# Optimization experiments

Measured on AMD Instinct MI355X. Metric: run time of the kernel, lower is better.

Reference implementation:

```python
import jax, jax.numpy as jnp
import numpy as np

N_ENT, N_REL, N_TRIG, N_ARGS = 100000, 250000, 50000, 250000
ENT_DIM, REL_R, RTYPE_DIM, ROLE_DIM, REL_SIZE = 288, 256, 32, 256, 200
ARG_DIM = REL_R + RTYPE_DIM + ENT_DIM  # 576


def setup_inputs() -> dict:
    key = jax.random.key(0)
    ks = jax.random.split(key, 11)
    s_in = 1.0 / np.sqrt(ARG_DIM)
    return {
        "ent_embeds": jax.random.normal(ks[0], (N_ENT, ENT_DIM), jnp.float32),
        "rel_embeds": jax.random.normal(ks[1], (N_REL, REL_R), jnp.float32),
        "rtype_table": jax.random.normal(ks[2], (REL_SIZE + 1, RTYPE_DIM), jnp.float32),
        "W_in": jax.random.normal(ks[3], (ARG_DIM, ROLE_DIM), jnp.float32) * s_in,
        "W_out": jax.random.normal(ks[4], (ARG_DIM, ROLE_DIM), jnp.float32) * s_in,
        "rtype_ids": jax.random.randint(ks[5], (N_REL,), 0, REL_SIZE, jnp.int32),
        "trig_ent_id": jax.random.randint(ks[6], (N_TRIG,), 0, N_ENT, jnp.int32),
        "arg_trig": jax.random.randint(ks[7], (N_ARGS,), 0, N_TRIG, jnp.int32),
        "arg_rel": jax.random.randint(ks[8], (N_ARGS,), 0, N_REL, jnp.int32),
        "arg_ent": jax.random.randint(ks[9], (N_ARGS,), 0, N_ENT, jnp.int32),
        "arg_is_in": jax.random.randint(ks[10], (N_ARGS,), 0, 2, jnp.int32),
    }


def reference(ent_embeds, rel_embeds, rtype_table, W_in, W_out,
              rtype_ids, trig_ent_id, arg_trig, arg_rel, arg_ent, arg_is_in):
    # per-relation type embedding (rtype_embedding_layer)
    rt_embeds = rtype_table[rtype_ids]                       # [N_REL, RTYPE_DIM]
    # per-argument gather + concat (get_arg_embeds): [rel | rtype | arg-entity]
    x = jnp.concatenate([rel_embeds[arg_rel],
                         rt_embeds[arg_rel],
                         ent_embeds[arg_ent]], axis=-1)      # [N_ARGS, ARG_DIM]
    # in_arg_layer vs out_arg_layer selected per argument (io_ids membership)
    m = arg_is_in.astype(x.dtype)[:, None]
    y = (x * m) @ W_in + (x * (1.0 - m)) @ W_out             # [N_ARGS, ROLE_DIM]
    # sum-aggregate per trigger (torch.sum over stacked arg embeds)
    args_sum = jax.ops.segment_sum(y, arg_trig, num_segments=N_TRIG)
    # concat trigger embedding with aggregated args (event_representation)
    return jnp.concatenate([ent_embeds[trig_ent_id], args_sum], axis=-1)  # [N_TRIG, ENT_DIM+ROLE_DIM]
```

## Files before the change

kernel.cpp:

```cpp
#include <hip/hip_runtime.h>
#include <hip/hip_bf16.h>
#include <stdint.h>

#define N_ENT    100000
#define N_REL    250000
#define N_TRIG   50000
#define N_ARGS   250000
#define ENT_DIM  288
#define REL_R    256
#define RTYPE_DIM 32
#define ROLE_DIM 256
#define ARG_DIM  576
#define OUT_DIM  544

#define BM 64
#define BK 32
#define NSTEP (ARG_DIM / BK)
#define LDP 40

typedef __attribute__((ext_vector_type(8))) short bf16x8;
typedef __attribute__((ext_vector_type(4))) float f32x4;

__device__ __forceinline__ short f2b(float f) {
    union { float f; uint32_t u; } v; v.f = f;
    uint32_t u = v.u;
    uint32_t r = (u + 0x7fffu + ((u >> 16) & 1u)) >> 16;
    return (short)r;
}

__global__ void __launch_bounds__(256)
k_init(const float* __restrict__ ent, const int* __restrict__ trig_ent,
       float* __restrict__ out)
{
    const int t   = blockIdx.x;
    const int tid = threadIdx.x;
    const int e   = trig_ent[t];
    const float* src = ent + (size_t)e * ENT_DIM;
    float*       dst = out + (size_t)t * OUT_DIM;
    dst[tid] = src[tid];
    if (tid < ENT_DIM - 256) dst[256 + tid] = src[256 + tid];
    dst[ENT_DIM + tid] = 0.f;
}

__global__ void __launch_bounds__(256)
k_prep(const float* __restrict__ W_in, const float* __restrict__ W_out,
       short* __restrict__ Wb)
{
    const int idx = blockIdx.x * 256 + threadIdx.x;
    const int w   = idx / (ARG_DIM * ROLE_DIM);
    const int rem = idx % (ARG_DIM * ROLE_DIM);
    const int k   = rem / ROLE_DIM;
    const int col = rem % ROLE_DIM;
    const float* src = (w == 0) ? W_in : W_out;
    Wb[((size_t)w * ROLE_DIM + col) * ARG_DIM + k] = f2b(src[k * ROLE_DIM + col]);
}

__global__ void __launch_bounds__(256)
k_gemm(const float* __restrict__ ent,  const float* __restrict__ rel,
       const float* __restrict__ rtab, const short* __restrict__ Wb,
       const int* __restrict__ rtype_ids, const int* __restrict__ arg_trig,
       const int* __restrict__ arg_rel,   const int* __restrict__ arg_ent,
       const int* __restrict__ arg_is_in, float* __restrict__ out)
{
    __shared__ short As[BM][LDP];
    __shared__ short Bi[ROLE_DIM][LDP];
    __shared__ short Bo[ROLE_DIM][LDP];
    __shared__ int s_rel[BM], s_ent[BM], s_rt[BM], s_trig[BM], s_mask[BM];

    const int tid = threadIdx.x;
    const int a0  = blockIdx.x * BM;

    if (tid < BM) {
        int a     = a0 + tid;
        int valid = (a < N_ARGS);
        int aa    = valid ? a : (N_ARGS - 1);
        int r     = arg_rel[aa];
        s_rel[tid]  = r;
        s_ent[tid]  = arg_ent[aa];
        s_rt[tid]   = rtype_ids[r];
        s_trig[tid] = arg_trig[aa];
        s_mask[tid] = valid ? arg_is_in[aa] : -1;
    }
    __syncthreads();

    const int lane  = tid & 63;
    const int wave  = tid >> 6;
    const int quad  = lane >> 4;
    const int l15   = lane & 15;
    const int nbase = wave * 64;

    int rowmask[4];
#pragma unroll
    for (int m = 0; m < 4; ++m) rowmask[m] = s_mask[m * 16 + l15];

    f32x4 acc[4][4];
#pragma unroll
    for (int m = 0; m < 4; ++m)
#pragma unroll
        for (int n = 0; n < 4; ++n) acc[m][n] = (f32x4){0.f, 0.f, 0.f, 0.f};

    const bf16x8 zf = {0, 0, 0, 0, 0, 0, 0, 0};

    const int srow = tid >> 2;
    const int skq  = (tid & 3) * 8;

    for (int s = 0; s < NSTEP; ++s) {
        __syncthreads();

        {
            const int k = s * BK + skq;
            const float* src;
            if (k < REL_R)
                src = rel + (size_t)s_rel[srow] * REL_R + k;
            else if (k < REL_R + RTYPE_DIM)
                src = rtab + s_rt[srow] * RTYPE_DIM + (k - REL_R);
            else
                src = ent + (size_t)s_ent[srow] * ENT_DIM + (k - REL_R - RTYPE_DIM);
            float4 v0 = *(const float4*)src;
            float4 v1 = *(const float4*)(src + 4);
            bf16x8 h;
            h[0] = f2b(v0.x); h[1] = f2b(v0.y); h[2] = f2b(v0.z); h[3] = f2b(v0.w);
            h[4] = f2b(v1.x); h[5] = f2b(v1.y); h[6] = f2b(v1.z); h[7] = f2b(v1.w);
            *(bf16x8*)&As[srow][skq] = h;
        }

        {
            const short* pin = Wb + (size_t)tid * ARG_DIM + s * BK;
            const short* pot = Wb + ((size_t)ROLE_DIM + tid) * ARG_DIM + s * BK;
#pragma unroll
            for (int j = 0; j < 4; ++j) {
                *(bf16x8*)&Bi[tid][j * 8] = *(const bf16x8*)(pin + j * 8);
                *(bf16x8*)&Bo[tid][j * 8] = *(const bf16x8*)(pot + j * 8);
            }
        }
        __syncthreads();

        bf16x8 a[4], bi[4], bo[4];
#pragma unroll
        for (int m = 0; m < 4; ++m)
            a[m] = *(const bf16x8*)&As[m * 16 + l15][quad * 8];
#pragma unroll
        for (int n = 0; n < 4; ++n) {
            bi[n] = *(const bf16x8*)&Bi[nbase + n * 16 + l15][quad * 8];
            bo[n] = *(const bf16x8*)&Bo[nbase + n * 16 + l15][quad * 8];
        }
#pragma unroll
        for (int m = 0; m < 4; ++m) {
            const bf16x8 ain = (rowmask[m] == 1) ? a[m] : zf;
            const bf16x8 aot = (rowmask[m] == 0) ? a[m] : zf;
#pragma unroll
            for (int n = 0; n < 4; ++n) {
                acc[m][n] = __builtin_amdgcn_mfma_f32_16x16x32_bf16(
                    ain, bi[n], acc[m][n], 0, 0, 0);
                acc[m][n] = __builtin_amdgcn_mfma_f32_16x16x32_bf16(
                    aot, bo[n], acc[m][n], 0, 0, 0);
            }
        }
    }

#pragma unroll
    for (int m = 0; m < 4; ++m) {
#pragma unroll
        for (int r4 = 0; r4 < 4; ++r4) {
            const int row = m * 16 + quad * 4 + r4;
            if (s_mask[row] < 0) continue;
            float* dst = out + (size_t)s_trig[row] * OUT_DIM + ENT_DIM;
#pragma unroll
            for (int n = 0; n < 4; ++n) {
                const int col = nbase + n * 16 + l15;
                atomicAdd(dst + col, acc[m][n][r4]);
            }
        }
    }
}

extern "C" void kernel_launch(void* const* d_in, const int* in_sizes, int n_in,
                              void* d_out, int out_size, void* d_ws, size_t ws_size,
                              hipStream_t stream)
{
    const float* ent      = (const float*)d_in[0];
    const float* rel      = (const float*)d_in[1];
    const float* rtab     = (const float*)d_in[2];
    const float* W_in     = (const float*)d_in[3];
    const float* W_out    = (const float*)d_in[4];
    const int*  rtype_ids = (const int*)d_in[5];
    const int*  trig_ent  = (const int*)d_in[6];
    const int*  arg_trig  = (const int*)d_in[7];
    const int*  arg_rel   = (const int*)d_in[8];
    const int*  arg_ent   = (const int*)d_in[9];
    const int*  arg_is_in = (const int*)d_in[10];

    float* out = (float*)d_out;
    short* Wb  = (short*)d_ws;

    hipLaunchKernelGGL(k_init, dim3(N_TRIG), dim3(256), 0, stream,
                       ent, trig_ent, out);
    hipLaunchKernelGGL(k_prep, dim3(2 * ARG_DIM * ROLE_DIM / 256), dim3(256), 0,
                       stream, W_in, W_out, Wb);
    hipLaunchKernelGGL(k_gemm, dim3((N_ARGS + BM - 1) / BM), dim3(256), 0, stream,
                       ent, rel, rtab, Wb,
                       rtype_ids, arg_trig, arg_rel, arg_ent, arg_is_in, out);
}
```

Measured before the change: 868.1 us.

## Restructure gather-GEMM with 512 threads, direct weight loads and register prefetch

The GEMM kernel moves to 512 threads per block, with each wave covering 32 output columns. Weight fragments are now read straight from global memory (L2-resident) instead of being staged through shared memory. The A-tile is double-buffered in LDS, and gathered rows are prefetched three steps ahead into registers, so there is one barrier per K step instead of two. The init kernel copies with float4 and handles four triggers per block. The aim is to cut LDS traffic and barrier stalls and to hide gather latency, at the cost of more global and L2 weight reads per wave.

```diff
diff --git a/kernel.cpp b/kernel.cpp
--- a/kernel.cpp
+++ b/kernel.cpp
@@ -19,6 +19,7 @@
 #define LDP 40
 
 typedef __attribute__((ext_vector_type(8))) short bf16x8;
+typedef __attribute__((ext_vector_type(4))) short bf16x4;
 typedef __attribute__((ext_vector_type(4))) float f32x4;
 
 __device__ __forceinline__ short f2b(float f) {
@@ -32,14 +33,15 @@
 k_init(const float* __restrict__ ent, const int* __restrict__ trig_ent,
        float* __restrict__ out)
 {
-    const int t   = blockIdx.x;
-    const int tid = threadIdx.x;
-    const int e   = trig_ent[t];
-    const float* src = ent + (size_t)e * ENT_DIM;
-    float*       dst = out + (size_t)t * OUT_DIM;
-    dst[tid] = src[tid];
-    if (tid < ENT_DIM - 256) dst[256 + tid] = src[256 + tid];
-    dst[ENT_DIM + tid] = 0.f;
+    const int t    = blockIdx.x * 4 + (threadIdx.x >> 6);
+    const int lane = threadIdx.x & 63;
+    const int e    = trig_ent[t];
+    const float4* src = (const float4*)(ent + (size_t)e * ENT_DIM);
+    float4*       dst = (float4*)(out + (size_t)t * OUT_DIM);
+    const float4 z = {0.f, 0.f, 0.f, 0.f};
+    dst[lane] = src[lane];
+    if (lane < 8) dst[64 + lane] = src[64 + lane];
+    dst[72 + lane] = z;
 }
 
 __global__ void __launch_bounds__(256)
@@ -55,16 +57,14 @@
     Wb[((size_t)w * ROLE_DIM + col) * ARG_DIM + k] = f2b(src[k * ROLE_DIM + col]);
 }
 
-__global__ void __launch_bounds__(256)
+__global__ void __launch_bounds__(512, 4)
 k_gemm(const float* __restrict__ ent,  const float* __restrict__ rel,
        const float* __restrict__ rtab, const short* __restrict__ Wb,
        const int* __restrict__ rtype_ids, const int* __restrict__ arg_trig,
        const int* __restrict__ arg_rel,   const int* __restrict__ arg_ent,
        const int* __restrict__ arg_is_in, float* __restrict__ out)
 {
-    __shared__ short As[BM][LDP];
-    __shared__ short Bi[ROLE_DIM][LDP];
-    __shared__ short Bo[ROLE_DIM][LDP];
+    __shared__ short As[2][BM][LDP];
     __shared__ int s_rel[BM], s_ent[BM], s_rt[BM], s_trig[BM], s_mask[BM];
 
     const int tid = threadIdx.x;
@@ -87,75 +87,78 @@
     const int wave  = tid >> 6;
     const int quad  = lane >> 4;
     const int l15   = lane & 15;
-    const int nbase = wave * 64;
+    const int nbase = wave * 32;
+
+    const int srow = tid >> 3;
+    const int skq  = (tid & 7) * 4;
+
+    const float* p_rel = rel  + (size_t)s_rel[srow] * REL_R    + skq;
+    const float* p_rt  = rtab + s_rt[srow] * RTYPE_DIM         + skq;
+    const float* p_ent = ent  + (size_t)s_ent[srow] * ENT_DIM  + skq;
+
+    const short* wbl = Wb + (size_t)(nbase + l15) * ARG_DIM + quad * 8;
 
     int rowmask[4];
 #pragma unroll
     for (int m = 0; m < 4; ++m) rowmask[m] = s_mask[m * 16 + l15];
 
-    f32x4 acc[4][4];
+    f32x4 acc[4][2];
 #pragma unroll
     for (int m = 0; m < 4; ++m)
 #pragma unroll
-        for (int n = 0; n < 4; ++n) acc[m][n] = (f32x4){0.f, 0.f, 0.f, 0.f};
+        for (int n = 0; n < 2; ++n) acc[m][n] = (f32x4){0.f, 0.f, 0.f, 0.f};
 
     const bf16x8 zf = {0, 0, 0, 0, 0, 0, 0, 0};
 
-    const int srow = tid >> 2;
-    const int skq  = (tid & 3) * 8;
-
-    for (int s = 0; s < NSTEP; ++s) {
-        __syncthreads();
-
-        {
-            const int k = s * BK + skq;
-            const float* src;
-            if (k < REL_R)
-                src = rel + (size_t)s_rel[srow] * REL_R + k;
-            else if (k < REL_R + RTYPE_DIM)
-                src = rtab + s_rt[srow] * RTYPE_DIM + (k - REL_R);
-            else
-                src = ent + (size_t)s_ent[srow] * ENT_DIM + (k - REL_R - RTYPE_DIM);
-            float4 v0 = *(const float4*)src;
-            float4 v1 = *(const float4*)(src + 4);
-            bf16x8 h;
-            h[0] = f2b(v0.x); h[1] = f2b(v0.y); h[2] = f2b(v0.z); h[3] = f2b(v0.w);
-            h[4] = f2b(v1.x); h[5] = f2b(v1.y); h[6] = f2b(v1.z); h[7] = f2b(v1.w);
-            *(bf16x8*)&As[srow][skq] = h;
-        }
-
-        {
-            const short* pin = Wb + (size_t)tid * ARG_DIM + s * BK;
-            const short* pot = Wb + ((size_t)ROLE_DIM + tid) * ARG_DIM + s * BK;
-#pragma unroll
-            for (int j = 0; j < 4; ++j) {
-                *(bf16x8*)&Bi[tid][j * 8] = *(const bf16x8*)(pin + j * 8);
-                *(bf16x8*)&Bo[tid][j * 8] = *(const bf16x8*)(pot + j * 8);
-            }
-        }
-        __syncthreads();
-
-        bf16x8 a[4], bi[4], bo[4];
+    float4 vA = *(const float4*)(p_rel);
+    float4 vB = *(const float4*)(p_rel + BK);
+    float4 vC = *(const float4*)(p_rel + 2 * BK);
+
+    auto STEP = [&](int s, float4& w) {
+        bf16x4 h;
+        h[0] = f2b(w.x); h[1] = f2b(w.y); h[2] = f2b(w.z); h[3] = f2b(w.w);
+        *(bf16x4*)&As[s & 1][srow][skq] = h;
+
+        asm volatile("s_waitcnt lgkmcnt(0)" ::: "memory");
+        __builtin_amdgcn_s_barrier();
+        asm volatile("" ::: "memory");
+
+        bf16x8 a[4];
 #pragma unroll
         for (int m = 0; m < 4; ++m)
-            a[m] = *(const bf16x8*)&As[m * 16 + l15][quad * 8];
-#pragma unroll
-        for (int n = 0; n < 4; ++n) {
-            bi[n] = *(const bf16x8*)&Bi[nbase + n * 16 + l15][quad * 8];
-            bo[n] = *(const bf16x8*)&Bo[nbase + n * 16 + l15][quad * 8];
-        }
+            a[m] = *(const bf16x8*)&As[s & 1][m * 16 + l15][quad * 8];
+
+        const short* bp = wbl + s * BK;
+        const bf16x8 bi0 = *(const bf16x8*)(bp);
+        const bf16x8 bi1 = *(const bf16x8*)(bp + 16 * ARG_DIM);
+        const bf16x8 bo0 = *(const bf16x8*)(bp + (size_t)ROLE_DIM * ARG_DIM);
+        const bf16x8 bo1 = *(const bf16x8*)(bp + (size_t)(ROLE_DIM + 16) * ARG_DIM);
+
 #pragma unroll
         for (int m = 0; m < 4; ++m) {
             const bf16x8 ain = (rowmask[m] == 1) ? a[m] : zf;
             const bf16x8 aot = (rowmask[m] == 0) ? a[m] : zf;
-#pragma unroll
-            for (int n = 0; n < 4; ++n) {
-                acc[m][n] = __builtin_amdgcn_mfma_f32_16x16x32_bf16(
-                    ain, bi[n], acc[m][n], 0, 0, 0);
-                acc[m][n] = __builtin_amdgcn_mfma_f32_16x16x32_bf16(
-                    aot, bo[n], acc[m][n], 0, 0, 0);
-            }
+            acc[m][0] = __builtin_amdgcn_mfma_f32_16x16x32_bf16(ain, bi0, acc[m][0], 0, 0, 0);
+            acc[m][0] = __builtin_amdgcn_mfma_f32_16x16x32_bf16(aot, bo0, acc[m][0], 0, 0, 0);
+            acc[m][1] = __builtin_amdgcn_mfma_f32_16x16x32_bf16(ain, bi1, acc[m][1], 0, 0, 0);
+            acc[m][1] = __builtin_amdgcn_mfma_f32_16x16x32_bf16(aot, bo1, acc[m][1], 0, 0, 0);
         }
+
+        __builtin_amdgcn_sched_barrier(0);
+        if (s + 3 < NSTEP) {
+            const int sn = s + 3;
+            const float* src = (sn < 8)  ? (p_rel + sn * BK)
+                             : (sn == 8) ? p_rt
+                                         : (p_ent + (sn - 9) * BK);
+            w = *(const float4*)src;
+        }
+    };
+
+#pragma unroll
+    for (int ss = 0; ss < NSTEP; ss += 3) {
+        STEP(ss,     vA);
+        STEP(ss + 1, vB);
+        STEP(ss + 2, vC);
     }
 
 #pragma unroll
@@ -164,12 +167,10 @@
         for (int r4 = 0; r4 < 4; ++r4) {
             const int row = m * 16 + quad * 4 + r4;
             if (s_mask[row] < 0) continue;
-            float* dst = out + (size_t)s_trig[row] * OUT_DIM + ENT_DIM;
-#pragma unroll
-            for (int n = 0; n < 4; ++n) {
-                const int col = nbase + n * 16 + l15;
-                atomicAdd(dst + col, acc[m][n][r4]);
-            }
+            float* dst = out + (size_t)s_trig[row] * OUT_DIM + ENT_DIM
+                             + nbase + l15;
+            atomicAdd(dst,      acc[m][0][r4]);
+            atomicAdd(dst + 16, acc[m][1][r4]);
         }
     }
 }
@@ -193,11 +194,11 @@
     float* out = (float*)d_out;
     short* Wb  = (short*)d_ws;
 
-    hipLaunchKernelGGL(k_init, dim3(N_TRIG), dim3(256), 0, stream,
+    hipLaunchKernelGGL(k_init, dim3(N_TRIG / 4), dim3(256), 0, stream,
                        ent, trig_ent, out);
     hipLaunchKernelGGL(k_prep, dim3(2 * ARG_DIM * ROLE_DIM / 256), dim3(256), 0,
                        stream, W_in, W_out, Wb);
-    hipLaunchKernelGGL(k_gemm, dim3((N_ARGS + BM - 1) / BM), dim3(256), 0, stream,
+    hipLaunchKernelGGL(k_gemm, dim3((N_ARGS + BM - 1) / BM), dim3(512), 0, stream,
                        ent, rel, rtab, Wb,
                        rtype_ids, arg_trig, arg_rel, arg_ent, arg_is_in, out);
 }
```

Result: faster. 832.4 us (-4.1%).
